# Performance work log

Measured on AMD Instinct MI355X. Metric: run time of the kernel, lower is better.

The kernel has to match this reference:

```python
import jax, jax.numpy as jnp
import numpy as np

B, S, D, H, DFF = 2, 2048, 768, 12, 3072
HD = D // H
LN_EPS = 1e-5


def _layernorm(x, g, b):
    mu = jnp.mean(x, axis=-1, keepdims=True)
    var = jnp.mean((x - mu) ** 2, axis=-1, keepdims=True)
    return (x - mu) * jax.lax.rsqrt(var + LN_EPS) * g + b


def setup_inputs() -> dict:
    key = jax.random.key(0)
    ks = jax.random.split(key, 16)
    s_d = 1.0 / np.sqrt(D)
    s_ff = 1.0 / np.sqrt(DFF)
    return {
        "x": jax.random.normal(ks[0], (B, S, D), jnp.float32),
        "alibi_bias": jax.random.normal(ks[1], (H, S, S), jnp.float32) * 0.1,
        "Wq": jax.random.normal(ks[2], (D, D), jnp.float32) * s_d,
        "bq": jnp.zeros((D,), jnp.float32),
        "Wk": jax.random.normal(ks[3], (D, D), jnp.float32) * s_d,
        "bk": jnp.zeros((D,), jnp.float32),
        "Wv": jax.random.normal(ks[4], (D, D), jnp.float32) * s_d,
        "bv": jnp.zeros((D,), jnp.float32),
        "Wo": jax.random.normal(ks[5], (D, D), jnp.float32) * s_d,
        "bo": jnp.zeros((D,), jnp.float32),
        "W1": jax.random.normal(ks[6], (D, DFF), jnp.float32) * s_d,
        "b1": jnp.zeros((DFF,), jnp.float32),
        "W2": jax.random.normal(ks[7], (DFF, D), jnp.float32) * s_ff,
        "b2": jnp.zeros((D,), jnp.float32),
        "g1": jnp.ones((D,), jnp.float32),
        "be1": jnp.zeros((D,), jnp.float32),
        "g2": jnp.ones((D,), jnp.float32),
        "be2": jnp.zeros((D,), jnp.float32),
    }


def reference(x, alibi_bias, Wq, bq, Wk, bk, Wv, bv, Wo, bo, W1, b1, W2, b2, g1, be1, g2, be2):
    # QKV projections -> (B, H, S, HD)
    def split_heads(t):
        return t.reshape(B, S, H, HD).transpose(0, 2, 1, 3)

    q = split_heads(x @ Wq + bq)
    k = split_heads(x @ Wk + bk)
    v = split_heads(x @ Wv + bv)

    # causal mask (S, S): -inf above diagonal
    causal = jnp.where(jnp.triu(jnp.ones((S, S), bool), k=1), -jnp.inf, 0.0).astype(x.dtype)
    mask = alibi_bias[None] + causal[None, None]  # (1, H, S, S) broadcast over batch

    scale = 1.0 / np.sqrt(HD)
    scores = jnp.einsum("bhqd,bhkd->bhqk", q, k) * scale + mask
    probs = jax.nn.softmax(scores, axis=-1)
    attn = jnp.einsum("bhqk,bhkd->bhqd", probs, v)  # (B, H, S, HD)
    attn = attn.transpose(0, 2, 1, 3).reshape(B, S, D)
    attn = attn @ Wo + bo

    x = _layernorm(x + attn, g1, be1)
    ff = jax.nn.relu(x @ W1 + b1) @ W2 + b2
    x = _layernorm(x + ff, g2, be2)
    return x
```

## Files before the change

kernel.cpp:

```cpp
#include <hip/hip_runtime.h>
#include <hip/hip_bf16.h>

#define BB 2
#define SS 2048
#define DD 768
#define HH 12
#define HD 64
#define DFF 3072
#define NROW (BB * SS)
#define QLD  2304
#define LN_EPS 1e-5f
#define NSPLIT 4

typedef __attribute__((ext_vector_type(8))) short bf16x8;
typedef __attribute__((ext_vector_type(4))) short bf16x4;
typedef __attribute__((ext_vector_type(4))) float f32x4;

__device__ __forceinline__ void gll16(const void* g, void* l) {
    __builtin_amdgcn_global_load_lds(
        (const __attribute__((address_space(1))) unsigned int*)g,
        (__attribute__((address_space(3))) unsigned int*)l,
        16, 0, 0);
}

__device__ __forceinline__ unsigned short bf16bits(float f) {
    __hip_bfloat16 h = __float2bfloat16(f);
    return *(unsigned short*)&h;
}

__device__ __forceinline__ float bf16tof(unsigned short u) {
    unsigned int ui = ((unsigned int)u) << 16;
    return __uint_as_float(ui);
}

__device__ __forceinline__ float block_sum(float v, float* red) {
    __syncthreads();
    #pragma unroll
    for (int off = 32; off > 0; off >>= 1) v += __shfl_down(v, off, 64);
    if ((threadIdx.x & 63) == 0) red[threadIdx.x >> 6] = v;
    __syncthreads();
    if (threadIdx.x == 0) red[0] = red[0] + red[1] + red[2] + red[3];
    __syncthreads();
    return red[0];
}

template<int TM, int TN>
__global__ __launch_bounds__(256) void mfma_gemm(
        const __hip_bfloat16* __restrict__ A, const __hip_bfloat16* __restrict__ BT,
        const float* __restrict__ bias, float* __restrict__ Cf,
        __hip_bfloat16* __restrict__ Cb,
        int N, int K, int relu, int bf16out, int qscale_cols) {
    constexpr int BK = 32;
    constexpr int MW = TM / 32;
    constexpr int NW = TN / 32;
    __shared__ __hip_bfloat16 a_s[TM * BK];
    __shared__ __hip_bfloat16 b_s[TN * BK];

    const int tid  = threadIdx.x;
    const int lane = tid & 63;
    const int wid  = tid >> 6;
    const int wm   = (wid & 1) * (TM / 2);
    const int wn   = (wid >> 1) * (TN / 2);
    const int qq   = lane & 15;
    const int quad = lane >> 4;
    const int m0 = blockIdx.y * TM;
    const int n0 = blockIdx.x * TN;

    const int srow = lane >> 2;
    const int scol = (lane & 3) * 8;

    f32x4 acc[MW][NW] = {};

    for (int k0 = 0; k0 < K; k0 += BK) {
        const __hip_bfloat16* Ag = A + (size_t)m0 * K + k0 + scol;
        #pragma unroll
        for (int i = 0; i < TM / 64; i++) {
            const int row = i * 64 + wid * 16 + srow;
            gll16(Ag + (size_t)row * K, a_s + row * BK + scol);
        }
        const __hip_bfloat16* Bg = BT + (size_t)n0 * K + k0 + scol;
        #pragma unroll
        for (int i = 0; i < TN / 64; i++) {
            const int row = i * 64 + wid * 16 + srow;
            gll16(Bg + (size_t)row * K, b_s + row * BK + scol);
        }
        __syncthreads();

        bf16x8 af[MW], bfr[NW];
        #pragma unroll
        for (int mi = 0; mi < MW; mi++)
            af[mi] = *(const bf16x8*)(a_s + (wm + mi * 16 + qq) * BK + quad * 8);
        #pragma unroll
        for (int ni = 0; ni < NW; ni++)
            bfr[ni] = *(const bf16x8*)(b_s + (wn + ni * 16 + qq) * BK + quad * 8);
        #pragma unroll
        for (int mi = 0; mi < MW; mi++)
            #pragma unroll
            for (int ni = 0; ni < NW; ni++)
                acc[mi][ni] = __builtin_amdgcn_mfma_f32_16x16x32_bf16(
                        af[mi], bfr[ni], acc[mi][ni], 0, 0, 0);
        __syncthreads();
    }

    #pragma unroll
    for (int mi = 0; mi < MW; mi++) {
        #pragma unroll
        for (int ni = 0; ni < NW; ni++) {
            const int col = n0 + wn + ni * 16 + qq;
            const float bv = bias[col];
            const float sc = (col < qscale_cols) ? 0.125f : 1.0f;
            #pragma unroll
            for (int r = 0; r < 4; r++) {
                const int row = m0 + wm + mi * 16 + quad * 4 + r;
                float v = acc[mi][ni][r] + bv;
                if (relu) v = fmaxf(v, 0.f);
                v *= sc;
                if (bf16out) Cb[(size_t)row * N + col] = __float2bfloat16(v);
                else         Cf[(size_t)row * N + col] = v;
            }
        }
    }
}

__device__ __forceinline__ void transpose_tile(
        const float* __restrict__ in, __hip_bfloat16* __restrict__ out,
        int K, int N, int tix, int tiy, float (*t)[33]) {
    const int n0 = tix * 32;
    const int k0 = tiy * 32;
    const int r = threadIdx.x >> 3;
    const int c = threadIdx.x & 7;
    float4 v = *(const float4*)&in[(size_t)(k0 + r) * N + n0 + c * 4];
    t[r][c * 4 + 0] = v.x;
    t[r][c * 4 + 1] = v.y;
    t[r][c * 4 + 2] = v.z;
    t[r][c * 4 + 3] = v.w;
    __syncthreads();
    union { unsigned short u[4]; uint2 w; } pk;
    #pragma unroll
    for (int j = 0; j < 4; j++) pk.u[j] = bf16bits(t[c * 4 + j][r]);
    *(uint2*)&out[(size_t)(n0 + r) * K + k0 + c * 4] = pk.w;
}

__global__ __launch_bounds__(256) void prep_kernel(
        const float* __restrict__ Wq, const float* __restrict__ Wk,
        const float* __restrict__ Wv, const float* __restrict__ Wo,
        const float* __restrict__ W1, const float* __restrict__ W2,
        const float* __restrict__ bq, const float* __restrict__ bk,
        const float* __restrict__ bv, const float* __restrict__ x,
        __hip_bfloat16* __restrict__ WqkvT, __hip_bfloat16* __restrict__ WoT,
        __hip_bfloat16* __restrict__ W1T, __hip_bfloat16* __restrict__ W2T,
        float* __restrict__ biasc, __hip_bfloat16* __restrict__ xb) {
    __shared__ float t[32][33];
    const int bx = blockIdx.x;
    if (bx < 2304) {
        const int wsel = bx / 576;
        const int r = bx - wsel * 576;
        const float* in = (wsel == 0) ? Wq : (wsel == 1) ? Wk : (wsel == 2) ? Wv : Wo;
        __hip_bfloat16* out = (wsel == 3) ? WoT : WqkvT + (size_t)wsel * DD * DD;
        transpose_tile(in, out, DD, DD, r % 24, r / 24, t);
    } else if (bx < 4608) {
        const int r = bx - 2304;
        transpose_tile(W1, W1T, DD, DFF, r % 96, r / 96, t);
    } else if (bx < 6912) {
        const int r = bx - 4608;
        transpose_tile(W2, W2T, DFF, DD, r % 24, r / 24, t);
    } else if (bx < 9984) {
        const int i = (bx - 6912) * 256 + threadIdx.x;
        float4 v = ((const float4*)x)[i];
        union { unsigned short u[4]; uint2 w; } pk;
        pk.u[0] = bf16bits(v.x); pk.u[1] = bf16bits(v.y);
        pk.u[2] = bf16bits(v.z); pk.u[3] = bf16bits(v.w);
        ((uint2*)xb)[i] = pk.w;
    } else {
        const int i = (bx - 9984) * 256 + threadIdx.x;
        if (i < QLD)
            biasc[i] = (i < DD) ? bq[i] : ((i < 2 * DD) ? bk[i - DD] : bv[i - 2 * DD]);
    }
}

__global__ __launch_bounds__(256) void flash_attn_kernel(
        const __hip_bfloat16* __restrict__ QKV, const float* __restrict__ alibi,
        __hip_bfloat16* __restrict__ Opart, float* __restrict__ ml) {
    const int qt = (int)(gridDim.x >> 2) - 1 - (int)(blockIdx.x >> 2);
    const int s  = blockIdx.x & 3;
    const int h  = blockIdx.y;
    const int b  = blockIdx.z;
    const int tid  = threadIdx.x;
    const int lane = tid & 63;
    const int w    = tid >> 6;
    const int qq   = lane & 15;
    const int quad = lane >> 4;
    const int q0   = qt * 64;

    __shared__ unsigned short K_s[64 * 72];
    __shared__ unsigned short V_t[64 * 72];
    __shared__ unsigned short al_q[64 * 72];
    __shared__ unsigned short P_t[4][16 * 72];

    const size_t qrow = ((size_t)(b * SS + q0 + w * 16 + qq)) * QLD + (size_t)h * HD;
    const bf16x8 qf0 = *(const bf16x8*)(QKV + qrow + quad * 8);
    const bf16x8 qf1 = *(const bf16x8*)(QKV + qrow + 32 + quad * 8);

    f32x4 O[4] = {};
    float m_i = -1e30f, l_i = 0.f;

    const float* alrow = alibi + ((size_t)h * SS + q0) * SS;
    const size_t kvrow0 = (size_t)(b * SS) * QLD + (size_t)h * HD + w * 16;
    const int lim = q0 + w * 16 + qq;

    for (int t = s; t * 64 <= q0; t += NSPLIT) {
        const int k0 = t * 64;
        __syncthreads();

        {
            const size_t kv = kvrow0 + (size_t)(k0 + lane) * QLD;
            bf16x8 kv0 = *(const bf16x8*)(QKV + DD + kv);
            bf16x8 kv1 = *(const bf16x8*)(QKV + DD + kv + 8);
            *(bf16x8*)&K_s[lane * 72 + w * 16]     = kv0;
            *(bf16x8*)&K_s[lane * 72 + w * 16 + 8] = kv1;
            bf16x8 vv0 = *(const bf16x8*)(QKV + 2 * DD + kv);
            bf16x8 vv1 = *(const bf16x8*)(QKV + 2 * DD + kv + 8);
            #pragma unroll
            for (int j = 0; j < 8; j++) {
                V_t[(w * 16 + j) * 72 + lane]     = vv0[j];
                V_t[(w * 16 + 8 + j) * 72 + lane] = vv1[j];
            }
            const float* ap = alrow + (size_t)lane * SS + k0 + w * 16;
            union { unsigned short u[8]; bf16x8 v; } pa0, pa1;
            float4 f0 = *(const float4*)(ap);
            float4 f1 = *(const float4*)(ap + 4);
            float4 f2 = *(const float4*)(ap + 8);
            float4 f3 = *(const float4*)(ap + 12);
            pa0.u[0] = bf16bits(f0.x); pa0.u[1] = bf16bits(f0.y);
            pa0.u[2] = bf16bits(f0.z); pa0.u[3] = bf16bits(f0.w);
            pa0.u[4] = bf16bits(f1.x); pa0.u[5] = bf16bits(f1.y);
            pa0.u[6] = bf16bits(f1.z); pa0.u[7] = bf16bits(f1.w);
            pa1.u[0] = bf16bits(f2.x); pa1.u[1] = bf16bits(f2.y);
            pa1.u[2] = bf16bits(f2.z); pa1.u[3] = bf16bits(f2.w);
            pa1.u[4] = bf16bits(f3.x); pa1.u[5] = bf16bits(f3.y);
            pa1.u[6] = bf16bits(f3.z); pa1.u[7] = bf16bits(f3.w);
            *(bf16x8*)&al_q[lane * 72 + w * 16]     = pa0.v;
            *(bf16x8*)&al_q[lane * 72 + w * 16 + 8] = pa1.v;
        }
        __syncthreads();

        f32x4 S[4];
        #pragma unroll
        for (int c = 0; c < 4; c++) {
            f32x4 sacc = {};
            bf16x8 kf0 = *(const bf16x8*)&K_s[(c * 16 + qq) * 72 + quad * 8];
            bf16x8 kf1 = *(const bf16x8*)&K_s[(c * 16 + qq) * 72 + 32 + quad * 8];
            sacc = __builtin_amdgcn_mfma_f32_16x16x32_bf16(kf0, qf0, sacc, 0, 0, 0);
            sacc = __builtin_amdgcn_mfma_f32_16x16x32_bf16(kf1, qf1, sacc, 0, 0, 0);
            S[c] = sacc;
        }

        float sv[16];
        float smax = -1e30f;
        const int klim = lim - k0;
        #pragma unroll
        for (int c = 0; c < 4; c++) {
            bf16x4 a4 = *(const bf16x4*)&al_q[(w * 16 + qq) * 72 + c * 16 + quad * 4];
            #pragma unroll
            for (int r = 0; r < 4; r++) {
                const int key = c * 16 + quad * 4 + r;
                float sc = S[c][r] + bf16tof((unsigned short)a4[r]);
                if (key > klim) sc = -1e30f;
                sv[c * 4 + r] = sc;
                smax = fmaxf(smax, sc);
            }
        }
        smax = fmaxf(smax, __shfl_xor(smax, 16));
        smax = fmaxf(smax, __shfl_xor(smax, 32));

        const float nm = fmaxf(m_i, smax);
        const float alpha = __expf(m_i - nm);
        float lsum = 0.f;
        #pragma unroll
        for (int i = 0; i < 16; i++) {
            const float e = __expf(sv[i] - nm);
            sv[i] = e;
            lsum += e;
        }
        lsum += __shfl_xor(lsum, 16);
        lsum += __shfl_xor(lsum, 32);
        l_i = l_i * alpha + lsum;
        m_i = nm;

        #pragma unroll
        for (int c = 0; c < 4; c++) {
            bf16x4 pk;
            #pragma unroll
            for (int r = 0; r < 4; r++) pk[r] = (short)bf16bits(sv[c * 4 + r]);
            *(bf16x4*)&P_t[w][qq * 72 + c * 16 + quad * 4] = pk;
        }

        #pragma unroll
        for (int r = 0; r < 4; r++) {
            const float ar = __shfl(alpha, quad * 4 + r);
            #pragma unroll
            for (int d = 0; d < 4; d++) O[d][r] *= ar;
        }

        const bf16x8 pf0 = *(const bf16x8*)&P_t[w][qq * 72 + quad * 8];
        const bf16x8 pf1 = *(const bf16x8*)&P_t[w][qq * 72 + 32 + quad * 8];
        #pragma unroll
        for (int d0 = 0; d0 < 4; d0++) {
            bf16x8 vf0 = *(const bf16x8*)&V_t[(d0 * 16 + qq) * 72 + quad * 8];
            bf16x8 vf1 = *(const bf16x8*)&V_t[(d0 * 16 + qq) * 72 + 32 + quad * 8];
            O[d0] = __builtin_amdgcn_mfma_f32_16x16x32_bf16(pf0, vf0, O[d0], 0, 0, 0);
            O[d0] = __builtin_amdgcn_mfma_f32_16x16x32_bf16(pf1, vf1, O[d0], 0, 0, 0);
        }
    }

    if (quad == 0) {
        float* mlp = ml + (((size_t)(b * SS + q0 + w * 16 + qq) * HH + h) * NSPLIT + s) * 2;
        mlp[0] = m_i;
        mlp[1] = l_i;
    }
    #pragma unroll
    for (int r = 0; r < 4; r++) {
        const int row = q0 + w * 16 + quad * 4 + r;
        __hip_bfloat16* op = Opart +
            (((size_t)(b * SS + row) * HH + h) * NSPLIT + s) * 64 + qq;
        op[0]  = __float2bfloat16(O[0][r]);
        op[16] = __float2bfloat16(O[1][r]);
        op[32] = __float2bfloat16(O[2][r]);
        op[48] = __float2bfloat16(O[3][r]);
    }
}

__global__ __launch_bounds__(256) void attn_combine_kernel(
        const __hip_bfloat16* __restrict__ Opart, const float* __restrict__ ml,
        __hip_bfloat16* __restrict__ attnb) {
    const int idx = blockIdx.x * 256 + threadIdx.x;
    const int rr  = idx / 96;
    const int rem = idx - rr * 96;
    const int h   = rem >> 3;
    const int d8  = (rem & 7) * 8;
    const size_t base = ((size_t)rr * HH + h) * NSPLIT;
    float ms[NSPLIT], ls[NSPLIT];
    float m = -1e30f;
    #pragma unroll
    for (int s = 0; s < NSPLIT; s++) {
        ms[s] = ml[(base + s) * 2];
        ls[s] = ml[(base + s) * 2 + 1];
        m = fmaxf(m, ms[s]);
    }
    float es[NSPLIT], denom = 0.f;
    #pragma unroll
    for (int s = 0; s < NSPLIT; s++) {
        es[s] = __expf(ms[s] - m);
        denom += ls[s] * es[s];
    }
    const float inv = 1.f / denom;
    float acc[8] = {};
    #pragma unroll
    for (int s = 0; s < NSPLIT; s++) {
        const bf16x8 o = *(const bf16x8*)(Opart + (base + s) * 64 + d8);
        #pragma unroll
        for (int j = 0; j < 8; j++)
            acc[j] += bf16tof((unsigned short)o[j]) * es[s];
    }
    union { unsigned short u[8]; bf16x8 v; } pk;
    #pragma unroll
    for (int j = 0; j < 8; j++) pk.u[j] = bf16bits(acc[j] * inv);
    *(bf16x8*)(attnb + (size_t)rr * DD + h * 64 + d8) = pk.v;
}

__global__ __launch_bounds__(256) void ln_kernel(
        const float* __restrict__ a, const float* __restrict__ r,
        const float* __restrict__ g, const float* __restrict__ beta,
        float* __restrict__ outf, __hip_bfloat16* __restrict__ outb) {
    const int row = blockIdx.x;
    const int tid = threadIdx.x;
    __shared__ float red[64];

    float vals[3];
    float s = 0.f;
    #pragma unroll
    for (int i = 0; i < 3; i++) {
        const int col = i * 256 + tid;
        float t = a[(size_t)row * DD + col] + r[(size_t)row * DD + col];
        vals[i] = t;
        s += t;
    }
    const float mean = block_sum(s, red) * (1.f / DD);

    float s2 = 0.f;
    #pragma unroll
    for (int i = 0; i < 3; i++) {
        float d = vals[i] - mean;
        s2 += d * d;
    }
    const float var = block_sum(s2, red) * (1.f / DD);
    const float rstd = rsqrtf(var + LN_EPS);

    #pragma unroll
    for (int i = 0; i < 3; i++) {
        const int col = i * 256 + tid;
        const float o = (vals[i] - mean) * rstd * g[col] + beta[col];
        outf[(size_t)row * DD + col] = o;
        if (outb) outb[(size_t)row * DD + col] = __float2bfloat16(o);
    }
}

extern "C" void kernel_launch(void* const* d_in, const int* in_sizes, int n_in,
                              void* d_out, int out_size, void* d_ws, size_t ws_size,
                              hipStream_t stream) {
    const float* x     = (const float*)d_in[0];
    const float* alibi = (const float*)d_in[1];
    const float* Wq = (const float*)d_in[2];
    const float* bq = (const float*)d_in[3];
    const float* Wk = (const float*)d_in[4];
    const float* bk = (const float*)d_in[5];
    const float* Wv = (const float*)d_in[6];
    const float* bv = (const float*)d_in[7];
    const float* Wo = (const float*)d_in[8];
    const float* bo = (const float*)d_in[9];
    const float* W1 = (const float*)d_in[10];
    const float* b1 = (const float*)d_in[11];
    const float* W2 = (const float*)d_in[12];
    const float* b2 = (const float*)d_in[13];
    const float* g1 = (const float*)d_in[14];
    const float* be1 = (const float*)d_in[15];
    const float* g2 = (const float*)d_in[16];
    const float* be2 = (const float*)d_in[17];
    float* out = (float*)d_out;

    char* p = (char*)d_ws;
    auto alloc = [&](size_t bytes) { char* r = p; p += (bytes + 255) & ~(size_t)255; return r; };
    __hip_bfloat16* WqkvT = (__hip_bfloat16*)alloc((size_t)QLD * DD * 2);
    __hip_bfloat16* WoT   = (__hip_bfloat16*)alloc((size_t)DD * DD * 2);
    __hip_bfloat16* W1T   = (__hip_bfloat16*)alloc((size_t)DFF * DD * 2);
    __hip_bfloat16* W2T   = (__hip_bfloat16*)alloc((size_t)DD * DFF * 2);
    float*          biasc = (float*)alloc((size_t)QLD * 4);
    __hip_bfloat16* xb    = (__hip_bfloat16*)alloc((size_t)NROW * DD * 2);
    __hip_bfloat16* qkvb  = (__hip_bfloat16*)alloc((size_t)NROW * DFF * 2);
    __hip_bfloat16* attnb = (__hip_bfloat16*)alloc((size_t)NROW * DD * 2);
    float*          proj  = (float*)alloc((size_t)NROW * DD * 4);
    float*          ln1   = (float*)alloc((size_t)NROW * DD * 4);
    __hip_bfloat16* ln1b  = xb;
    __hip_bfloat16* ff1b  = qkvb;
    float*          ff2   = proj;

    __hip_bfloat16* Opart = (__hip_bfloat16*)proj;
    float*          mlbuf = (float*)xb;

    const dim3 blk(256);

    prep_kernel<<<dim3(9993), blk, 0, stream>>>(
            Wq, Wk, Wv, Wo, W1, W2, bq, bk, bv, x,
            WqkvT, WoT, W1T, W2T, biasc, xb);

    mfma_gemm<128, 128><<<dim3(QLD / 128, NROW / 128), blk, 0, stream>>>(
            xb, WqkvT, biasc, nullptr, qkvb, QLD, DD, 0, 1, DD);

    flash_attn_kernel<<<dim3(NSPLIT * (SS / 64), HH, BB), blk, 0, stream>>>(
            qkvb, alibi, Opart, mlbuf);
    attn_combine_kernel<<<dim3(NROW * 96 / 256), blk, 0, stream>>>(
            Opart, mlbuf, attnb);

    mfma_gemm<128, 64><<<dim3(DD / 64, NROW / 128), blk, 0, stream>>>(
            attnb, WoT, bo, proj, nullptr, DD, DD, 0, 0, 0);

    ln_kernel<<<dim3(NROW), blk, 0, stream>>>(x, proj, g1, be1, ln1, ln1b);

    mfma_gemm<128, 128><<<dim3(DFF / 128, NROW / 128), blk, 0, stream>>>(
            ln1b, W1T, b1, nullptr, ff1b, DFF, DD, 1, 1, 0);
    mfma_gemm<128, 64><<<dim3(DD / 64, NROW / 128), blk, 0, stream>>>(
            ff1b, W2T, b2, ff2, nullptr, DD, DFF, 0, 0, 0);

    ln_kernel<<<dim3(NROW), blk, 0, stream>>>(ln1, ff2, g2, be2, out, nullptr);
}
```

Baseline: 539.9 us.

## Double GEMM K-tile with XOR-swizzled LDS, read alibi directly, add MFMA priority hints

The GEMM K tile grows from 32 to 64, and the LDS layout is XOR-swizzled to avoid bank conflicts, with two MFMA k-steps per tile. In flash attention, the alibi bias is no longer staged through shared memory as bf16. Each lane now reads its fp32 bias values straight from global memory after the barrier, which also keeps full bias precision. s_setprio hints are placed around the MFMA blocks to favour matrix issue across waves. Together these cut barriers, LDS traffic and conversion work, at the cost of more LDS per GEMM block and possibly less coalesced alibi reads.

After: 499.0 us. -7.6%, faster.

```diff
diff --git a/kernel.cpp b/kernel.cpp
--- a/kernel.cpp
+++ b/kernel.cpp
@@ -50,7 +50,7 @@
         const float* __restrict__ bias, float* __restrict__ Cf,
         __hip_bfloat16* __restrict__ Cb,
         int N, int K, int relu, int bf16out, int qscale_cols) {
-    constexpr int BK = 32;
+    constexpr int BK = 64;
     constexpr int MW = TM / 32;
     constexpr int NW = TN / 32;
     __shared__ __hip_bfloat16 a_s[TM * BK];
@@ -66,39 +66,48 @@
     const int m0 = blockIdx.y * TM;
     const int n0 = blockIdx.x * TN;
 
-    const int srow = lane >> 2;
-    const int scol = (lane & 3) * 8;
+    const int r8   = lane >> 3;
+    const int u8   = lane & 7;
+    const int gcol = ((u8 ^ r8) << 3);
 
     f32x4 acc[MW][NW] = {};
 
     for (int k0 = 0; k0 < K; k0 += BK) {
-        const __hip_bfloat16* Ag = A + (size_t)m0 * K + k0 + scol;
-        #pragma unroll
-        for (int i = 0; i < TM / 64; i++) {
-            const int row = i * 64 + wid * 16 + srow;
-            gll16(Ag + (size_t)row * K, a_s + row * BK + scol);
-        }
-        const __hip_bfloat16* Bg = BT + (size_t)n0 * K + k0 + scol;
-        #pragma unroll
-        for (int i = 0; i < TN / 64; i++) {
-            const int row = i * 64 + wid * 16 + srow;
-            gll16(Bg + (size_t)row * K, b_s + row * BK + scol);
+        const __hip_bfloat16* Ag = A + (size_t)m0 * K + k0 + gcol;
+        #pragma unroll
+        for (int i = 0; i < TM / 32; i++) {
+            const int row = i * 32 + wid * 8 + r8;
+            gll16(Ag + (size_t)row * K, a_s + row * BK + u8 * 8);
+        }
+        const __hip_bfloat16* Bg = BT + (size_t)n0 * K + k0 + gcol;
+        #pragma unroll
+        for (int i = 0; i < TN / 32; i++) {
+            const int row = i * 32 + wid * 8 + r8;
+            gll16(Bg + (size_t)row * K, b_s + row * BK + u8 * 8);
         }
         __syncthreads();
 
-        bf16x8 af[MW], bfr[NW];
-        #pragma unroll
-        for (int mi = 0; mi < MW; mi++)
-            af[mi] = *(const bf16x8*)(a_s + (wm + mi * 16 + qq) * BK + quad * 8);
-        #pragma unroll
-        for (int ni = 0; ni < NW; ni++)
-            bfr[ni] = *(const bf16x8*)(b_s + (wn + ni * 16 + qq) * BK + quad * 8);
-        #pragma unroll
-        for (int mi = 0; mi < MW; mi++)
-            #pragma unroll
-            for (int ni = 0; ni < NW; ni++)
-                acc[mi][ni] = __builtin_amdgcn_mfma_f32_16x16x32_bf16(
-                        af[mi], bfr[ni], acc[mi][ni], 0, 0, 0);
+        #pragma unroll
+        for (int kh = 0; kh < 2; kh++) {
+            const int ku = kh * 4 + quad;
+            bf16x8 af[MW], bfr[NW];
+            #pragma unroll
+            for (int mi = 0; mi < MW; mi++) {
+                const int row = wm + mi * 16 + qq;
+                af[mi] = *(const bf16x8*)(a_s + row * BK + ((ku ^ (qq & 7)) << 3));
+            }
+            #pragma unroll
+            for (int ni = 0; ni < NW; ni++) {
+                const int row = wn + ni * 16 + qq;
+                bfr[ni] = *(const bf16x8*)(b_s + row * BK + ((ku ^ (qq & 7)) << 3));
+            }
+            #pragma unroll
+            for (int mi = 0; mi < MW; mi++)
+                #pragma unroll
+                for (int ni = 0; ni < NW; ni++)
+                    acc[mi][ni] = __builtin_amdgcn_mfma_f32_16x16x32_bf16(
+                            af[mi], bfr[ni], acc[mi][ni], 0, 0, 0);
+        }
         __syncthreads();
     }
 
@@ -194,7 +203,6 @@
 
     __shared__ unsigned short K_s[64 * 72];
     __shared__ unsigned short V_t[64 * 72];
-    __shared__ unsigned short al_q[64 * 72];
     __shared__ unsigned short P_t[4][16 * 72];
 
     const size_t qrow = ((size_t)(b * SS + q0 + w * 16 + qq)) * QLD + (size_t)h * HD;
@@ -204,7 +212,7 @@
     f32x4 O[4] = {};
     float m_i = -1e30f, l_i = 0.f;
 
-    const float* alrow = alibi + ((size_t)h * SS + q0) * SS;
+    const float* alrow = alibi + ((size_t)h * SS + q0 + w * 16 + qq) * SS;
     const size_t kvrow0 = (size_t)(b * SS) * QLD + (size_t)h * HD + w * 16;
     const int lim = q0 + w * 16 + qq;
 
@@ -225,25 +233,15 @@
                 V_t[(w * 16 + j) * 72 + lane]     = vv0[j];
                 V_t[(w * 16 + 8 + j) * 72 + lane] = vv1[j];
             }
-            const float* ap = alrow + (size_t)lane * SS + k0 + w * 16;
-            union { unsigned short u[8]; bf16x8 v; } pa0, pa1;
-            float4 f0 = *(const float4*)(ap);
-            float4 f1 = *(const float4*)(ap + 4);
-            float4 f2 = *(const float4*)(ap + 8);
-            float4 f3 = *(const float4*)(ap + 12);
-            pa0.u[0] = bf16bits(f0.x); pa0.u[1] = bf16bits(f0.y);
-            pa0.u[2] = bf16bits(f0.z); pa0.u[3] = bf16bits(f0.w);
-            pa0.u[4] = bf16bits(f1.x); pa0.u[5] = bf16bits(f1.y);
-            pa0.u[6] = bf16bits(f1.z); pa0.u[7] = bf16bits(f1.w);
-            pa1.u[0] = bf16bits(f2.x); pa1.u[1] = bf16bits(f2.y);
-            pa1.u[2] = bf16bits(f2.z); pa1.u[3] = bf16bits(f2.w);
-            pa1.u[4] = bf16bits(f3.x); pa1.u[5] = bf16bits(f3.y);
-            pa1.u[6] = bf16bits(f3.z); pa1.u[7] = bf16bits(f3.w);
-            *(bf16x8*)&al_q[lane * 72 + w * 16]     = pa0.v;
-            *(bf16x8*)&al_q[lane * 72 + w * 16 + 8] = pa1.v;
         }
         __syncthreads();
 
+        float4 av[4];
+        #pragma unroll
+        for (int c = 0; c < 4; c++)
+            av[c] = *(const float4*)(alrow + k0 + c * 16 + quad * 4);
+
+        __builtin_amdgcn_s_setprio(1);
         f32x4 S[4];
         #pragma unroll
         for (int c = 0; c < 4; c++) {
@@ -254,17 +252,17 @@
             sacc = __builtin_amdgcn_mfma_f32_16x16x32_bf16(kf1, qf1, sacc, 0, 0, 0);
             S[c] = sacc;
         }
+        __builtin_amdgcn_s_setprio(0);
 
         float sv[16];
         float smax = -1e30f;
         const int klim = lim - k0;
         #pragma unroll
         for (int c = 0; c < 4; c++) {
-            bf16x4 a4 = *(const bf16x4*)&al_q[(w * 16 + qq) * 72 + c * 16 + quad * 4];
             #pragma unroll
             for (int r = 0; r < 4; r++) {
                 const int key = c * 16 + quad * 4 + r;
-                float sc = S[c][r] + bf16tof((unsigned short)a4[r]);
+                float sc = S[c][r] + ((const float*)&av[c])[r];
                 if (key > klim) sc = -1e30f;
                 sv[c * 4 + r] = sc;
                 smax = fmaxf(smax, sc);
@@ -304,6 +302,7 @@
 
         const bf16x8 pf0 = *(const bf16x8*)&P_t[w][qq * 72 + quad * 8];
         const bf16x8 pf1 = *(const bf16x8*)&P_t[w][qq * 72 + 32 + quad * 8];
+        __builtin_amdgcn_s_setprio(1);
         #pragma unroll
         for (int d0 = 0; d0 < 4; d0++) {
             bf16x8 vf0 = *(const bf16x8*)&V_t[(d0 * 16 + qq) * 72 + quad * 8];
@@ -311,6 +310,7 @@
             O[d0] = __builtin_amdgcn_mfma_f32_16x16x32_bf16(pf0, vf0, O[d0], 0, 0, 0);
             O[d0] = __builtin_amdgcn_mfma_f32_16x16x32_bf16(pf1, vf1, O[d0], 0, 0, 0);
         }
+        __builtin_amdgcn_s_setprio(0);
     }
 
     if (quad == 0) {
```
